# Kernel optimization log

Measured on AMD Instinct MI355X. Metric: run time of the kernel, lower is better.

The kernel has to match this reference:

```python
import jax, jax.numpy as jnp
import numpy as np

B = 256
LSTM = 512
FEAT = 3 * 3 * 512 + 16 + 8  # 4632
N_ACT = 4
ACT_SHAPE = 64
NUM_STEPS = 20
CANVAS_IN = 6 * 32 * 32  # 6144
H1 = int(FEAT / (FEAT / LSTM) ** (1.0 / 3.0))  # 2223
H2 = int(FEAT / (FEAT / LSTM) ** (2.0 / 3.0))  # 1067


def setup_inputs() -> dict:
    key = jax.random.key(0)
    ks = jax.random.split(key, 32)

    def g(k, shape, scale=0.02):
        return jax.random.normal(k, shape, dtype=jnp.float32) * scale

    inp = {
        "actualCanvas": jax.random.normal(ks[0], (B, 3, 32, 32), dtype=jnp.float32),
        "objectiveCanvas": jax.random.normal(ks[1], (B, 3, 32, 32), dtype=jnp.float32),
        "last_action_end_position": jax.random.randint(ks[2], (B,), 0, ACT_SHAPE),
        "episode_percentage": jax.random.randint(ks[3], (B,), 0, NUM_STEPS),
        # feature extractor stub (flatten -> linear -> relu), output 4608
        "Wfe": g(ks[4], (4608, CANVAS_IN)), "bfe": jnp.zeros((4608,), jnp.float32),
        "emb_end": g(ks[5], (ACT_SHAPE, 16), 1.0),
        "emb_ep": g(ks[6], (NUM_STEPS, 8), 1.0),
        "W1": g(ks[7], (H1, FEAT)), "b1": jnp.zeros((H1,), jnp.float32),
        "W2": g(ks[8], (H2, H1)), "b2": jnp.zeros((H2,), jnp.float32),
        "W3": g(ks[9], (LSTM, H2)), "b3": jnp.zeros((LSTM,), jnp.float32),
        "W_ih": g(ks[10], (4 * LSTM, LSTM)), "W_hh": g(ks[11], (4 * LSTM, LSTM)),
        "b_ih": jnp.zeros((4 * LSTM,), jnp.float32), "b_hh": jnp.zeros((4 * LSTM,), jnp.float32),
        "Wd1": g(ks[12], (N_ACT, LSTM // 2, LSTM)), "bd1": jnp.zeros((N_ACT, LSTM // 2), jnp.float32),
        "Wd2": g(ks[13], (N_ACT, ACT_SHAPE, LSTM // 2)), "bd2": jnp.zeros((N_ACT, ACT_SHAPE), jnp.float32),
        "emb_dec": g(ks[14], (N_ACT, ACT_SHAPE, 16), 1.0),
        "Wout": g(ks[15], (LSTM, LSTM + 16)), "bout": jnp.zeros((LSTM,), jnp.float32),
    }
    return inp


def reference(actualCanvas, objectiveCanvas, last_action_end_position, episode_percentage,
              Wfe, bfe, emb_end, emb_ep, W1, b1, W2, b2, W3, b3,
              W_ih, W_hh, b_ih, b_hh, Wd1, bd1, Wd2, bd2, emb_dec, Wout, bout):
    # feature extractor on channel-concatenated canvases -> [B, 4608]
    x = jnp.concatenate([actualCanvas, objectiveCanvas], axis=1).reshape(B, -1)
    fv = jax.nn.relu(x @ Wfe.T + bfe)
    feats = jnp.concatenate([fv, emb_end[last_action_end_position], emb_ep[episode_percentage]], axis=1)
    # fc1->fc2->fc3 (dropout = eval mode / identity)
    h = jax.nn.relu(feats @ W1.T + b1)
    h = jax.nn.relu(h @ W2.T + b2)
    h = jax.nn.relu(h @ W3.T + b3)  # [B, LSTM]
    # single-step LSTM with zero initial state (first execution)
    gates = h @ W_ih.T + b_ih + b_hh  # h0 = 0 so recurrent matmul vanishes
    i, f, g_, o = jnp.split(gates, 4, axis=1)
    c = jax.nn.sigmoid(i) * jnp.tanh(g_)
    seed = jax.nn.sigmoid(o) * jnp.tanh(c)  # [B, LSTM]
    z = seed
    log_probabilities = jnp.zeros((B,), jnp.float32)
    entropy = jnp.float32(0.0)
    actions = []
    base_key = jax.random.key(42)
    for k in range(N_ACT):
        hm = jax.nn.relu(z @ Wd1[k].T + bd1[k])
        logits = hm @ Wd2[k].T + bd2[k]  # [B, ACT_SHAPE]
        logp = jax.nn.log_softmax(logits, axis=1)
        probs = jnp.exp(logp)
        entropy = entropy + jnp.sum(-probs * logp)
        act = jax.random.categorical(jax.random.fold_in(base_key, k), logits, axis=1)  # [B]
        actions.append(act)
        log_probabilities = log_probabilities + jnp.take_along_axis(logp, act[:, None], axis=1)[:, 0]
        emb_a = emb_dec[k][act]  # [B,16]
        z = jax.nn.relu(jnp.concatenate([z, emb_a], axis=1) @ Wout.T + bout)
    action = jnp.stack(actions, axis=1)  # [B, N_ACT]
    return action, entropy, log_probabilities
```

## Files before the change

### kernel.cpp

```cpp
#include <hip/hip_runtime.h>
#include <hip/hip_bf16.h>
#include <stdint.h>

#define B_SZ   256
#define LSTM_N 512
#define FEAT_N 4632
#define FV_N   4608
#define CIN_N  6144
#define HALF_CIN 3072
#define ACT_N  64
#define LDSW   72
#define LD_FEAT 4672
#define LD_ZEXT 576

typedef __attribute__((ext_vector_type(8))) short bf16x8;
typedef __attribute__((ext_vector_type(4))) float f32x4;

#define BARRIER() asm volatile("s_waitcnt lgkmcnt(0)\ns_barrier" ::: "memory")

__device__ __forceinline__ short f2bf(float f) {
  uint32_t u = __float_as_uint(f);
  u += 0x7FFFu + ((u >> 16) & 1u);
  return (short)(u >> 16);
}
__device__ __forceinline__ float bf2f(short s) {
  return __uint_as_float(((uint32_t)(uint16_t)s) << 16);
}

__device__ __forceinline__ uint32_t rotl32(uint32_t x, int r) {
  return (x << r) | (x >> (32 - r));
}
__device__ __forceinline__ void threefry2x32(uint32_t k0, uint32_t k1,
                                             uint32_t x0, uint32_t x1,
                                             uint32_t& o0, uint32_t& o1) {
  uint32_t k2 = k0 ^ k1 ^ 0x1BD11BDAu;
  x0 += k0; x1 += k1;
  x0 += x1; x1 = rotl32(x1, 13); x1 ^= x0;
  x0 += x1; x1 = rotl32(x1, 15); x1 ^= x0;
  x0 += x1; x1 = rotl32(x1, 26); x1 ^= x0;
  x0 += x1; x1 = rotl32(x1,  6); x1 ^= x0;
  x0 += k1; x1 += k2 + 1u;
  x0 += x1; x1 = rotl32(x1, 17); x1 ^= x0;
  x0 += x1; x1 = rotl32(x1, 29); x1 ^= x0;
  x0 += x1; x1 = rotl32(x1, 16); x1 ^= x0;
  x0 += x1; x1 = rotl32(x1, 24); x1 ^= x0;
  x0 += k2; x1 += k0 + 2u;
  x0 += x1; x1 = rotl32(x1, 13); x1 ^= x0;
  x0 += x1; x1 = rotl32(x1, 15); x1 ^= x0;
  x0 += x1; x1 = rotl32(x1, 26); x1 ^= x0;
  x0 += x1; x1 = rotl32(x1,  6); x1 ^= x0;
  x0 += k0; x1 += k1 + 3u;
  x0 += x1; x1 = rotl32(x1, 17); x1 ^= x0;
  x0 += x1; x1 = rotl32(x1, 29); x1 ^= x0;
  x0 += x1; x1 = rotl32(x1, 16); x1 ^= x0;
  x0 += x1; x1 = rotl32(x1, 24); x1 ^= x0;
  x0 += k1; x1 += k2 + 4u;
  x0 += x1; x1 = rotl32(x1, 13); x1 ^= x0;
  x0 += x1; x1 = rotl32(x1, 15); x1 ^= x0;
  x0 += x1; x1 = rotl32(x1, 26); x1 ^= x0;
  x0 += x1; x1 = rotl32(x1,  6); x1 ^= x0;
  x0 += k2; x1 += k0 + 5u;
  o0 = x0; o1 = x1;
}

__global__ void concat_cvt_kernel(const float* __restrict__ act,
                                  const float* __restrict__ obj,
                                  short* __restrict__ xb) {
  int idx = blockIdx.x * 256 + threadIdx.x;
  if (idx >= B_SZ * 768) return;
  int row = idx / 768;
  int c8 = (idx - row * 768) * 8;
  const float* src = (c8 < HALF_CIN) ? (act + (size_t)row * HALF_CIN + c8)
                                     : (obj + (size_t)row * HALF_CIN + (c8 - HALF_CIN));
  float4 u = ((const float4*)src)[0];
  float4 v = ((const float4*)src)[1];
  bf16x8 r;
  r[0]=f2bf(u.x); r[1]=f2bf(u.y); r[2]=f2bf(u.z); r[3]=f2bf(u.w);
  r[4]=f2bf(v.x); r[5]=f2bf(v.y); r[6]=f2bf(v.z); r[7]=f2bf(v.w);
  *(bf16x8*)&xb[(size_t)row * CIN_N + c8] = r;
}

__global__ void gumbel_kernel(float* __restrict__ gum) {
  int idx = blockIdx.x * 256 + threadIdx.x;
  if (idx >= 4 * 16384) return;
  int k = idx >> 14;
  uint32_t j = (uint32_t)(idx & 16383);
  uint32_t f0, f1, o0, o1, bits;
  threefry2x32(0u, 42u, 0u, (uint32_t)k, f0, f1);
  if (j < 8192u) { threefry2x32(f0, f1, j, j + 8192u, o0, o1); bits = o0; }
  else           { threefry2x32(f0, f1, j - 8192u, j, o0, o1); bits = o1; }
  const float tiny = 1.17549435e-38f;
  float fu = __uint_as_float((bits >> 9) | 0x3f800000u) - 1.0f;
  float u = fmaxf(tiny, fu * (1.0f - tiny) + tiny);
  gum[idx] = -logf(-logf(u));
}

__global__ void fill_embs_kernel(const int* __restrict__ lastpos,
                                 const int* __restrict__ ep,
                                 const float* __restrict__ emb_end,
                                 const float* __restrict__ emb_ep,
                                 short* __restrict__ feats) {
  int b = blockIdx.x;
  int t = threadIdx.x;
  short* row = feats + (size_t)b * LD_FEAT;
  if (t < 16)      row[FV_N + t] = f2bf(emb_end[lastpos[b] * 16 + t]);
  else if (t < 24) row[FV_N + 16 + (t - 16)] = f2bf(emb_ep[ep[b] * 8 + (t - 16)]);
  else             row[FV_N + t] = 0;
}

__global__ __launch_bounds__(512) void gemm3_kernel(
    const short* __restrict__ A, int ldab,
    const float* __restrict__ W, int ldw,
    const float* __restrict__ bias1, const float* __restrict__ bias2,
    void* __restrict__ Cout, int ldc,
    short* __restrict__ P,
    int N, int K, int do_relu, int mode_f32, int kc, int nchunks) {
  __shared__ short Wlds[2][64 * LDSW];

  const int tid = threadIdx.x;
  const int w = tid >> 6, l = tid & 63, l15 = l & 15, lg = l >> 4;
  const int n0 = blockIdx.x * 64;
  const int Np = gridDim.x * 64;
  const int ks = blockIdx.y;
  const int kbeg = ks * kc;
  const int kend = (kbeg + kc < K) ? (kbeg + kc) : K;
  const int nk = (kend - kbeg + 63) >> 6;
  const bool wfast = ((ldw & 3) == 0);

  f32x4 acc[2][4];
#pragma unroll
  for (int i = 0; i < 2; ++i)
#pragma unroll
    for (int j = 0; j < 4; ++j) acc[i][j] = (f32x4){0.f, 0.f, 0.f, 0.f};

  const int wrow = tid >> 3, wq = tid & 7;
  float4 wrA[2], wrB[2], wrC[2], wrD[2];
  bf16x8 a0[4], a1[4];

  auto loadW = [&](float4* dst, int k0) {
    int gn = n0 + wrow; if (gn >= N) gn = N - 1;
    int gk = k0 + (wq << 3);
    const float* p = W + (size_t)gn * ldw + gk;
    if (wfast && (k0 + 64 <= K)) {
      dst[0] = ((const float4*)p)[0];
      dst[1] = ((const float4*)p)[1];
    } else {
      float t[8];
#pragma unroll
      for (int j = 0; j < 8; ++j) t[j] = (gk + j < K) ? p[j] : 0.f;
      dst[0] = (float4){t[0], t[1], t[2], t[3]};
      dst[1] = (float4){t[4], t[5], t[6], t[7]};
    }
  };
  auto storeW = [&](const float4* src, int buf) {
    short4 s0, s1;
    s0.x = f2bf(src[0].x); s0.y = f2bf(src[0].y);
    s0.z = f2bf(src[0].z); s0.w = f2bf(src[0].w);
    s1.x = f2bf(src[1].x); s1.y = f2bf(src[1].y);
    s1.z = f2bf(src[1].z); s1.w = f2bf(src[1].w);
    short* q = &Wlds[buf][wrow * LDSW + (wq << 3)];
    *(short4*)q = s0;
    *(short4*)(q + 4) = s1;
  };
  auto loadA = [&](bf16x8* dst, int k0) {
#pragma unroll
    for (int mi = 0; mi < 2; ++mi)
#pragma unroll
      for (int kh = 0; kh < 2; ++kh) {
        int m = (w << 5) + (mi << 4) + l15;
        int kk = k0 + (kh << 5) + (lg << 3);
        dst[(mi << 1) + kh] = *(const bf16x8*)&A[(size_t)m * ldab + kk];
      }
  };

#define MFMA_STEP(ACUR, BUF)                                                        \
  {                                                                                 \
    _Pragma("unroll")                                                               \
    for (int nj = 0; nj < 4; ++nj) {                                                \
      const short* bp = &Wlds[BUF][((nj << 4) + l15) * LDSW + (lg << 3)];           \
      bf16x8 b0 = *(const bf16x8*)bp;                                               \
      bf16x8 b1 = *(const bf16x8*)(bp + 32);                                        \
      acc[0][nj] = __builtin_amdgcn_mfma_f32_16x16x32_bf16(ACUR[0], b0, acc[0][nj], 0, 0, 0); \
      acc[1][nj] = __builtin_amdgcn_mfma_f32_16x16x32_bf16(ACUR[2], b0, acc[1][nj], 0, 0, 0); \
      acc[0][nj] = __builtin_amdgcn_mfma_f32_16x16x32_bf16(ACUR[1], b1, acc[0][nj], 0, 0, 0); \
      acc[1][nj] = __builtin_amdgcn_mfma_f32_16x16x32_bf16(ACUR[3], b1, acc[1][nj], 0, 0, 0); \
    }                                                                               \
  }

#define KSTEP(KT, WISS, WST, AC, AN, BUFC, BUFN)                      \
  {                                                                   \
    if ((KT) + 4 < nk) loadW(WISS, kbeg + (((KT) + 4) << 6));         \
    if ((KT) + 1 < nk) loadA(AN, kbeg + (((KT) + 1) << 6));           \
    MFMA_STEP(AC, BUFC);                                              \
    if ((KT) + 1 < nk) { storeW(WST, BUFN); BARRIER(); }              \
  }

  loadW(wrA, kbeg);
  if (nk > 1) loadW(wrB, kbeg + 64);
  if (nk > 2) loadW(wrC, kbeg + 128);
  if (nk > 3) loadW(wrD, kbeg + 192);
  loadA(a0, kbeg);
  storeW(wrA, 0);
  BARRIER();

  for (int kt = 0; kt < nk; kt += 4) {
    KSTEP(kt, wrA, wrB, a0, a1, 0, 1);
    if (kt + 1 < nk) KSTEP(kt + 1, wrB, wrC, a1, a0, 1, 0);
    if (kt + 2 < nk) KSTEP(kt + 2, wrC, wrD, a0, a1, 0, 1);
    if (kt + 3 < nk) KSTEP(kt + 3, wrD, wrA, a1, a0, 1, 0);
  }
#undef KSTEP
#undef MFMA_STEP

  if (nchunks == 1 && Cout) {
#pragma unroll
    for (int nj = 0; nj < 4; ++nj) {
      int gn = n0 + (nj << 4) + l15;
      float bsum = 0.f;
      if (gn < N) {
        if (bias1) bsum += bias1[gn];
        if (bias2) bsum += bias2[gn];
      }
#pragma unroll
      for (int mi = 0; mi < 2; ++mi)
#pragma unroll
        for (int r = 0; r < 4; ++r) {
          int gm = (w << 5) + (mi << 4) + (lg << 2) + r;
          float v = (gn < N) ? (acc[mi][nj][r] + bsum) : 0.f;
          if (do_relu) v = fmaxf(v, 0.f);
          if (mode_f32) ((float*)Cout)[(size_t)gm * ldc + gn] = v;
          else          ((short*)Cout)[(size_t)gm * ldc + gn] = f2bf(v);
        }
    }
  } else {
    short* Pb = P + (size_t)ks * 256 * Np;
#pragma unroll
    for (int nj = 0; nj < 4; ++nj) {
      int gn = n0 + (nj << 4) + l15;
#pragma unroll
      for (int mi = 0; mi < 2; ++mi)
#pragma unroll
        for (int r = 0; r < 4; ++r) {
          int gm = (w << 5) + (mi << 4) + (lg << 2) + r;
          Pb[(size_t)gm * Np + gn] = f2bf(acc[mi][nj][r]);
        }
    }
  }
}

__global__ void reduce_kernel(const short* __restrict__ P, int Np, int nchunks,
                              const float* __restrict__ bias1,
                              const float* __restrict__ bias2,
                              void* __restrict__ out, int ldc, int N,
                              int relu, int mode_f32) {
  int npack = Np >> 3;
  int idx = blockIdx.x * 256 + threadIdx.x;
  if (idx >= 256 * npack) return;
  int m = idx / npack;
  int n8 = (idx - m * npack) << 3;
  float s[8] = {0.f, 0.f, 0.f, 0.f, 0.f, 0.f, 0.f, 0.f};
  for (int ks = 0; ks < nchunks; ++ks) {
    bf16x8 v = *(const bf16x8*)&P[(size_t)ks * 256 * Np + (size_t)m * Np + n8];
#pragma unroll
    for (int j = 0; j < 8; ++j) s[j] += bf2f(v[j]);
  }
#pragma unroll
  for (int j = 0; j < 8; ++j) {
    int n = n8 + j;
    float r = 0.f;
    if (n < N) {
      r = s[j];
      if (bias1) r += bias1[n];
      if (bias2) r += bias2[n];
      if (relu) r = fmaxf(r, 0.f);
    }
    s[j] = r;
  }
  if (mode_f32) {
    float* o = (float*)out + (size_t)m * ldc + n8;
#pragma unroll
    for (int j = 0; j < 8; ++j) o[j] = s[j];
  } else {
    bf16x8 r;
#pragma unroll
    for (int j = 0; j < 8; ++j) r[j] = f2bf(s[j]);
    *(bf16x8*)((short*)out + (size_t)m * ldc + n8) = r;
  }
}

__global__ void reduce_lstm_kernel(const short* __restrict__ P, int nchunks,
                                   const float* __restrict__ b_ih,
                                   const float* __restrict__ b_hh,
                                   short* __restrict__ zext) {
  int idx = blockIdx.x * 256 + threadIdx.x;
  if (idx >= 256 * 64) return;
  int m = idx >> 6;
  int n8 = (idx & 63) << 3;
  float gi[8] = {}, gg[8] = {}, go[8] = {};
  for (int ks = 0; ks < nchunks; ++ks) {
    const short* base = P + ((size_t)ks * 256 + m) * 2048;
    bf16x8 vi = *(const bf16x8*)(base + n8);
    bf16x8 vg = *(const bf16x8*)(base + 1024 + n8);
    bf16x8 vo = *(const bf16x8*)(base + 1536 + n8);
#pragma unroll
    for (int j = 0; j < 8; ++j) {
      gi[j] += bf2f(vi[j]); gg[j] += bf2f(vg[j]); go[j] += bf2f(vo[j]);
    }
  }
  bf16x8 hv;
#pragma unroll
  for (int j = 0; j < 8; ++j) {
    int n = n8 + j;
    float i_ = gi[j] + b_ih[n] + b_hh[n];
    float g_ = gg[j] + b_ih[1024 + n] + b_hh[1024 + n];
    float o_ = go[j] + b_ih[1536 + n] + b_hh[1536 + n];
    float si = 1.f / (1.f + expf(-i_));
    float so = 1.f / (1.f + expf(-o_));
    float c = si * tanhf(g_);
    hv[j] = f2bf(so * tanhf(c));
  }
  *(bf16x8*)&zext[(size_t)m * LD_ZEXT + n8] = hv;
}

__global__ __launch_bounds__(256) void logits_sample_kernel(
    const short* __restrict__ hm,
    const float* __restrict__ Wd2k,
    const float* __restrict__ bd2k,
    const float* __restrict__ gumk,
    const float* __restrict__ embk,
    short* __restrict__ zext,
    int* __restrict__ act_out, float* __restrict__ logp_out,
    float* __restrict__ ent_out, int write_emb) {
  __shared__ short Wl[64 * 264];
  const int tid = threadIdx.x;
  const int w = tid >> 6, l = tid & 63, l15 = l & 15, lg = l >> 4;
  const int mbase = blockIdx.x * 64 + w * 16;

  {
    int r = tid >> 2;
    int c0 = (tid & 3) << 6;
    const float* src = Wd2k + r * 256 + c0;
    short* dst = &Wl[r * 264 + c0];
#pragma unroll
    for (int i = 0; i < 8; ++i) {
      float4 u = ((const float4*)src)[2 * i];
      float4 v = ((const float4*)src)[2 * i + 1];
      bf16x8 t;
      t[0]=f2bf(u.x); t[1]=f2bf(u.y); t[2]=f2bf(u.z); t[3]=f2bf(u.w);
      t[4]=f2bf(v.x); t[5]=f2bf(v.y); t[6]=f2bf(v.z); t[7]=f2bf(v.w);
      *(bf16x8*)(dst + 8 * i) = t;
    }
  }
  __syncthreads();

  f32x4 acc[4];
#pragma unroll
  for (int j = 0; j < 4; ++j) acc[j] = (f32x4){0.f, 0.f, 0.f, 0.f};

#pragma unroll
  for (int kt = 0; kt < 4; ++kt) {
    int k0 = kt << 6;
    const short* arow = &hm[(size_t)(mbase + l15) * 256 + k0 + (lg << 3)];
    bf16x8 af0 = *(const bf16x8*)arow;
    bf16x8 af1 = *(const bf16x8*)(arow + 32);
#pragma unroll
    for (int nj = 0; nj < 4; ++nj) {
      const short* bp = &Wl[((nj << 4) + l15) * 264 + k0 + (lg << 3)];
      bf16x8 b0 = *(const bf16x8*)bp;
      bf16x8 b1 = *(const bf16x8*)(bp + 32);
      acc[nj] = __builtin_amdgcn_mfma_f32_16x16x32_bf16(af0, b0, acc[nj], 0, 0, 0);
      acc[nj] = __builtin_amdgcn_mfma_f32_16x16x32_bf16(af1, b1, acc[nj], 0, 0, 0);
    }
  }

  float bcol[4];
#pragma unroll
  for (int nj = 0; nj < 4; ++nj) bcol[nj] = bd2k[(nj << 4) + l15];

#pragma unroll
  for (int r = 0; r < 4; ++r) {
    int row = mbase + (lg << 2) + r;
    float lv[4];
#pragma unroll
    for (int nj = 0; nj < 4; ++nj) lv[nj] = acc[nj][r] + bcol[nj];
    float mx = fmaxf(fmaxf(lv[0], lv[1]), fmaxf(lv[2], lv[3]));
#pragma unroll
    for (int off = 8; off; off >>= 1) mx = fmaxf(mx, __shfl_xor(mx, off));
    float es = expf(lv[0]-mx) + expf(lv[1]-mx) + expf(lv[2]-mx) + expf(lv[3]-mx);
#pragma unroll
    for (int off = 8; off; off >>= 1) es += __shfl_xor(es, off);
    float lse = logf(es);
    float lp[4], ent = 0.f;
#pragma unroll
    for (int nj = 0; nj < 4; ++nj) {
      lp[nj] = lv[nj] - mx - lse;
      ent += -expf(lp[nj]) * lp[nj];
    }
#pragma unroll
    for (int off = 8; off; off >>= 1) ent += __shfl_xor(ent, off);
    float bv = -3.4e38f; int bc = 64; float blp = 0.f;
#pragma unroll
    for (int nj = 0; nj < 4; ++nj) {
      int col = (nj << 4) + l15;
      float pert = lv[nj] + gumk[row * 64 + col];
      if (pert > bv || (pert == bv && col < bc)) { bv = pert; bc = col; blp = lp[nj]; }
    }
#pragma unroll
    for (int off = 8; off; off >>= 1) {
      float ov = __shfl_xor(bv, off);
      int oc = __shfl_xor(bc, off);
      float olp = __shfl_xor(blp, off);
      if (ov > bv || (ov == bv && oc < bc)) { bv = ov; bc = oc; blp = olp; }
    }
    if (l15 == 0) {
      act_out[row] = bc;
      logp_out[row] = blp;
      ent_out[row] = ent;
    }
    if (write_emb) {
      short* zr = zext + (size_t)row * LD_ZEXT;
      zr[512 + l15] = f2bf(embk[bc * 16 + l15]);
      zr[528 + l15] = 0;
      zr[544 + l15] = 0;
      zr[560 + l15] = 0;
    }
  }
}

__global__ void finalize_kernel(const int* __restrict__ act,
                                const float* __restrict__ logp_k,
                                const float* __restrict__ ent,
                                float* __restrict__ out) {
  __shared__ float sred[4];
  int t = threadIdx.x;
#pragma unroll
  for (int k = 0; k < 4; ++k)
    out[t * 4 + k] = (float)act[k * 256 + t];
  float lp = 0.f;
#pragma unroll
  for (int k = 0; k < 4; ++k) lp += logp_k[k * 256 + t];
  out[1025 + t] = lp;

  float v = 0.f;
#pragma unroll
  for (int k = 0; k < 4; ++k) v += ent[k * 256 + t];
#pragma unroll
  for (int off = 32; off; off >>= 1) v += __shfl_xor(v, off);
  if ((t & 63) == 0) sred[t >> 6] = v;
  __syncthreads();
  if (t == 0) out[1024] = sred[0] + sred[1] + sred[2] + sred[3];
}

extern "C" void kernel_launch(void* const* d_in, const int* in_sizes, int n_in,
                              void* d_out, int out_size, void* d_ws, size_t ws_size,
                              hipStream_t stream) {
  float* out = (float*)d_out;
  char* out_bytes = (char*)d_out;
  auto sentinel = [&](int code) { hipMemsetAsync(out_bytes + 4096, code, 4, stream); };

  if (n_in < 25 || in_sizes[0] != B_SZ * 3 * 32 * 32 ||
      in_sizes[4] != FV_N * CIN_N || in_sizes[23] != LSTM_N * 528 ||
      in_sizes[9] <= 0 || in_sizes[9] > 8192 ||
      in_sizes[11] <= 0 || in_sizes[11] > 8192) {
    sentinel(0x42);
    return;
  }

  const float* actual = (const float*)d_in[0];
  const float* object = (const float*)d_in[1];
  const int* lastpos  = (const int*)d_in[2];
  const int* ep       = (const int*)d_in[3];
  const float* Wfe    = (const float*)d_in[4];
  const float* bfe    = (const float*)d_in[5];
  const float* emb_end= (const float*)d_in[6];
  const float* emb_ep = (const float*)d_in[7];
  const float* W1     = (const float*)d_in[8];
  const float* b1     = (const float*)d_in[9];
  const float* W2     = (const float*)d_in[10];
  const float* b2     = (const float*)d_in[11];
  const float* W3     = (const float*)d_in[12];
  const float* b3     = (const float*)d_in[13];
  const float* W_ih   = (const float*)d_in[14];
  const float* b_ih   = (const float*)d_in[16];
  const float* b_hh   = (const float*)d_in[17];
  const float* Wd1    = (const float*)d_in[18];
  const float* bd1    = (const float*)d_in[19];
  const float* Wd2    = (const float*)d_in[20];
  const float* bd2    = (const float*)d_in[21];
  const float* embdec = (const float*)d_in[22];
  const float* Wout   = (const float*)d_in[23];
  const float* bout   = (const float*)d_in[24];

  const int H1 = in_sizes[9];
  const int H2 = in_sizes[11];
  const int ldh1 = 64 * ((H1 + 63) / 64);
  const int ldh2 = 64 * ((H2 + 63) / 64);

  char* wsb = (char*)d_ws;
  size_t off = 0;
  auto alloc = [&](size_t bytes) {
    char* p = wsb + off;
    off += (bytes + 255) & ~(size_t)255;
    return p;
  };
  float* logpk = (float*)alloc(1024 * 4);
  float* entk  = (float*)alloc(1024 * 4);
  int*   actk  = (int*)alloc(1024 * 4);
  float* gumb  = (float*)alloc(4 * 16384 * 4);
  short* xb    = (short*)alloc((size_t)B_SZ * CIN_N * 2);
  short* feats = (short*)alloc((size_t)B_SZ * LD_FEAT * 2);
  short* h1    = (short*)alloc((size_t)B_SZ * ldh1 * 2);
  short* h2    = (short*)alloc((size_t)B_SZ * ldh2 * 2);
  short* h3    = (short*)alloc((size_t)B_SZ * 512 * 2);
  short* zextA = (short*)alloc((size_t)B_SZ * LD_ZEXT * 2);
  short* zextB = (short*)alloc((size_t)B_SZ * LD_ZEXT * 2);
  short* hm    = (short*)alloc((size_t)B_SZ * 256 * 2);
  if (off + (4 << 20) > ws_size) {
    sentinel(0x43);
    return;
  }
  short* slab = (short*)(wsb + off);
  const size_t slab_bytes = ws_size - off;

  auto gemm = [&](const short* A, int ldab, const float* W, int ldw,
                  const float* bb1, const float* bb2,
                  void* C, int ldc, int N, int K, int relu, int mode_f32,
                  bool split, int fuse) {
    int nblk = (N + 63) / 64;
    int Np = nblk * 64;
    int chunks = 1;
    int kc = 64 * ((K + 63) / 64);
    if (split) {
      int c = (640 + nblk - 1) / nblk;
      int capk = K >> 7; if (capk < 1) capk = 1;
      if (c > capk) c = capk;
      size_t cap = slab_bytes / ((size_t)256 * Np * 2);
      if ((size_t)c > cap) c = (int)cap;
      if (c < 1) c = 1;
      kc = 64 * ((K + 64 * c - 1) / (64 * c));
      chunks = (K + kc - 1) / kc;
    }
    dim3 g(nblk, chunks);
    void* Ck = (fuse == 1) ? nullptr : C;
    gemm3_kernel<<<g, dim3(512), 0, stream>>>(
        A, ldab, W, ldw, bb1, bb2, Ck, ldc, slab, N, K, relu, mode_f32, kc, chunks);
    if (fuse == 1) {
      reduce_lstm_kernel<<<dim3(64), dim3(256), 0, stream>>>(
          slab, chunks, bb1, bb2, (short*)C);
    } else if (chunks > 1) {
      int npack = Np >> 3;
      reduce_kernel<<<dim3((256 * npack + 255) / 256), dim3(256), 0, stream>>>(
          slab, Np, chunks, bb1, bb2, C, ldc, N, relu, mode_f32);
    }
  };

  concat_cvt_kernel<<<dim3(768), dim3(256), 0, stream>>>(actual, object, xb);
  gumbel_kernel<<<dim3(256), dim3(256), 0, stream>>>(gumb);
  gemm(xb, CIN_N, Wfe, CIN_N, bfe, nullptr, feats, LD_FEAT, FV_N, CIN_N, 1, 0, true, 0);
  fill_embs_kernel<<<dim3(B_SZ), dim3(64), 0, stream>>>(lastpos, ep, emb_end, emb_ep, feats);
  gemm(feats, LD_FEAT, W1, FEAT_N, b1, nullptr, h1, ldh1, H1, FEAT_N, 1, 0, true, 0);
  gemm(h1, ldh1, W2, H1, b2, nullptr, h2, ldh2, H2, H1, 1, 0, true, 0);
  gemm(h2, ldh2, W3, H2, b3, nullptr, h3, 512, LSTM_N, H2, 1, 0, true, 0);
  gemm(h3, 512, W_ih, LSTM_N, b_ih, b_hh, zextA, LD_ZEXT, 4 * LSTM_N, LSTM_N, 0, 0, true, 1);

  short* zcur = zextA;
  short* znxt = zextB;
  for (int k = 0; k < 4; ++k) {
    const float* Wd1k = Wd1 + (size_t)k * 256 * LSTM_N;
    const float* bd1k = bd1 + (size_t)k * 256;
    const float* Wd2k = Wd2 + (size_t)k * ACT_N * 256;
    const float* bd2k = bd2 + (size_t)k * ACT_N;
    const float* embk = embdec + (size_t)k * ACT_N * 16;
    gemm(zcur, LD_ZEXT, Wd1k, LSTM_N, bd1k, nullptr, hm, 256, 256, LSTM_N, 1, 0, false, 0);
    logits_sample_kernel<<<dim3(4), dim3(256), 0, stream>>>(
        hm, Wd2k, bd2k, gumb + k * 16384, embk, zcur,
        actk + k * B_SZ, logpk + k * B_SZ, entk + k * B_SZ, (k < 3) ? 1 : 0);
    if (k < 3) {
      gemm(zcur, LD_ZEXT, Wout, 528, bout, nullptr, znxt, LD_ZEXT, LSTM_N, 528, 1, 0, false, 0);
      short* t = zcur; zcur = znxt; znxt = t;
    }
  }

  finalize_kernel<<<dim3(1), dim3(256), 0, stream>>>(actk, logpk, entk, out);
}
```

Measured before the change: 319.8 us.

## Restructure GEMM K-loop into four-buffer LDS batches and retune split-K

Replaces the double-buffered LDS weight pipeline, which stored one tile and hit a barrier after every 64-wide K step, with a four-buffer scheme. Four weight tiles are prefetched into registers, four MFMA steps run from LDS, and all four tiles are then stored between two barriers. This cuts barriers per K step. The cost is more LDS per block, which may lower occupancy, and a longer stall at each batch boundary. The split-K heuristic also changes to target more blocks with larger minimum chunks (K>>8 cap), so each chunk spans enough K tiles to fill the batches.

Result: faster. 310.1 us (-3.0%).

```diff
diff --git a/kernel.cpp b/kernel.cpp
--- a/kernel.cpp
+++ b/kernel.cpp
@@ -115,7 +115,7 @@
     void* __restrict__ Cout, int ldc,
     short* __restrict__ P,
     int N, int K, int do_relu, int mode_f32, int kc, int nchunks) {
-  __shared__ short Wlds[2][64 * LDSW];
+  __shared__ short Wlds[4][64 * LDSW];
 
   const int tid = threadIdx.x;
   const int w = tid >> 6, l = tid & 63, l15 = l & 15, lg = l >> 4;
@@ -134,7 +134,7 @@
     for (int j = 0; j < 4; ++j) acc[i][j] = (f32x4){0.f, 0.f, 0.f, 0.f};
 
   const int wrow = tid >> 3, wq = tid & 7;
-  float4 wrA[2], wrB[2], wrC[2], wrD[2];
+  float4 wr0[2], wr1[2], wr2[2], wr3[2];
   bf16x8 a0[4], a1[4];
 
   auto loadW = [&](float4* dst, int k0) {
@@ -187,29 +187,47 @@
     }                                                                               \
   }
 
-#define KSTEP(KT, WISS, WST, AC, AN, BUFC, BUFN)                      \
-  {                                                                   \
-    if ((KT) + 4 < nk) loadW(WISS, kbeg + (((KT) + 4) << 6));         \
-    if ((KT) + 1 < nk) loadA(AN, kbeg + (((KT) + 1) << 6));           \
-    MFMA_STEP(AC, BUFC);                                              \
-    if ((KT) + 1 < nk) { storeW(WST, BUFN); BARRIER(); }              \
-  }
-
-  loadW(wrA, kbeg);
-  if (nk > 1) loadW(wrB, kbeg + 64);
-  if (nk > 2) loadW(wrC, kbeg + 128);
-  if (nk > 3) loadW(wrD, kbeg + 192);
+  if (0 < nk) loadW(wr0, kbeg);
+  if (1 < nk) loadW(wr1, kbeg + 64);
+  if (2 < nk) loadW(wr2, kbeg + 128);
+  if (3 < nk) loadW(wr3, kbeg + 192);
   loadA(a0, kbeg);
-  storeW(wrA, 0);
+  if (0 < nk) storeW(wr0, 0);
+  if (1 < nk) storeW(wr1, 1);
+  if (2 < nk) storeW(wr2, 2);
+  if (3 < nk) storeW(wr3, 3);
   BARRIER();
 
-  for (int kt = 0; kt < nk; kt += 4) {
-    KSTEP(kt, wrA, wrB, a0, a1, 0, 1);
-    if (kt + 1 < nk) KSTEP(kt + 1, wrB, wrC, a1, a0, 1, 0);
-    if (kt + 2 < nk) KSTEP(kt + 2, wrC, wrD, a0, a1, 0, 1);
-    if (kt + 3 < nk) KSTEP(kt + 3, wrD, wrA, a1, a0, 1, 0);
-  }
-#undef KSTEP
+  for (int b = 0; b < nk; b += 4) {
+    if (b + 4 < nk) loadW(wr0, kbeg + ((b + 4) << 6));
+    if (b + 5 < nk) loadW(wr1, kbeg + ((b + 5) << 6));
+    if (b + 6 < nk) loadW(wr2, kbeg + ((b + 6) << 6));
+    if (b + 7 < nk) loadW(wr3, kbeg + ((b + 7) << 6));
+    {
+      if (b + 1 < nk) loadA(a1, kbeg + ((b + 1) << 6));
+      MFMA_STEP(a0, 0);
+    }
+    if (b + 1 < nk) {
+      if (b + 2 < nk) loadA(a0, kbeg + ((b + 2) << 6));
+      MFMA_STEP(a1, 1);
+    }
+    if (b + 2 < nk) {
+      if (b + 3 < nk) loadA(a1, kbeg + ((b + 3) << 6));
+      MFMA_STEP(a0, 2);
+    }
+    if (b + 3 < nk) {
+      if (b + 4 < nk) loadA(a0, kbeg + ((b + 4) << 6));
+      MFMA_STEP(a1, 3);
+    }
+    if (b + 4 < nk) {
+      BARRIER();
+      storeW(wr0, 0);
+      if (b + 5 < nk) storeW(wr1, 1);
+      if (b + 6 < nk) storeW(wr2, 2);
+      if (b + 7 < nk) storeW(wr3, 3);
+      BARRIER();
+    }
+  }
 #undef MFMA_STEP
 
   if (nchunks == 1 && Cout) {
@@ -531,8 +549,8 @@
     int chunks = 1;
     int kc = 64 * ((K + 63) / 64);
     if (split) {
-      int c = (640 + nblk - 1) / nblk;
-      int capk = K >> 7; if (capk < 1) capk = 1;
+      int c = (768 + nblk - 1) / nblk;
+      int capk = K >> 8; if (capk < 1) capk = 1;
       if (c > capk) c = capk;
       size_t cap = slab_bytes / ((size_t)256 * Np * 2);
       if ((size_t)c > cap) c = (int)cap;
```

## Replace LDS-staged GEMM with register-direct weight loads and wider split-K

Applied to the files above, without the earlier changes.

The GEMM kernel no longer stages fp32 weights through double-buffered LDS with barriers. Each wave now loads and converts its weight fragments straight from global memory into registers and computes a 64x64 tile with 4 waves of 256 threads. The split-K target rises from 640 to 1536 blocks and the chunk count is now capped by the number of K tiles. The small decoder GEMMs also switch to split-K with a separate reduce pass. This is meant to remove barrier and LDS overhead and raise parallelism for the bandwidth-bound weight streaming. The cost is that each wave rereads the weight rows with no prefetch pipelining, and extra reduce launches are added for the tiny decoder GEMMs.

Result: slower. 377.6 us (+18.1%).

```diff
diff --git a/kernel.cpp b/kernel.cpp
--- a/kernel.cpp
+++ b/kernel.cpp
@@ -9,14 +9,11 @@
 #define CIN_N  6144
 #define HALF_CIN 3072
 #define ACT_N  64
-#define LDSW   72
 #define LD_FEAT 4672
 #define LD_ZEXT 576
 
 typedef __attribute__((ext_vector_type(8))) short bf16x8;
 typedef __attribute__((ext_vector_type(4))) float f32x4;
-
-#define BARRIER() asm volatile("s_waitcnt lgkmcnt(0)\ns_barrier" ::: "memory")
 
 __device__ __forceinline__ short f2bf(float f) {
   uint32_t u = __float_as_uint(f);
@@ -108,109 +105,73 @@
   else             row[FV_N + t] = 0;
 }
 
-__global__ __launch_bounds__(512) void gemm3_kernel(
+__global__ __launch_bounds__(256, 3) void gemm4_kernel(
     const short* __restrict__ A, int ldab,
     const float* __restrict__ W, int ldw,
     const float* __restrict__ bias1, const float* __restrict__ bias2,
     void* __restrict__ Cout, int ldc,
     short* __restrict__ P,
     int N, int K, int do_relu, int mode_f32, int kc, int nchunks) {
-  __shared__ short Wlds[2][64 * LDSW];
-
   const int tid = threadIdx.x;
-  const int w = tid >> 6, l = tid & 63, l15 = l & 15, lg = l >> 4;
+  const int wv = tid >> 6, l = tid & 63, l15 = l & 15, lg = l >> 4;
   const int n0 = blockIdx.x * 64;
   const int Np = gridDim.x * 64;
   const int ks = blockIdx.y;
   const int kbeg = ks * kc;
   const int kend = (kbeg + kc < K) ? (kbeg + kc) : K;
-  const int nk = (kend - kbeg + 63) >> 6;
-  const bool wfast = ((ldw & 3) == 0);
-
-  f32x4 acc[2][4];
-#pragma unroll
-  for (int i = 0; i < 2; ++i)
+  const bool wal = ((ldw & 3) == 0);
+  const int mrow = wv << 6;
+
+  f32x4 acc[4][4];
+#pragma unroll
+  for (int i = 0; i < 4; ++i)
 #pragma unroll
     for (int j = 0; j < 4; ++j) acc[i][j] = (f32x4){0.f, 0.f, 0.f, 0.f};
 
-  const int wrow = tid >> 3, wq = tid & 7;
-  float4 wrA[2], wrB[2], wrC[2], wrD[2];
-  bf16x8 a0[4], a1[4];
-
-  auto loadW = [&](float4* dst, int k0) {
-    int gn = n0 + wrow; if (gn >= N) gn = N - 1;
-    int gk = k0 + (wq << 3);
-    const float* p = W + (size_t)gn * ldw + gk;
-    if (wfast && (k0 + 64 <= K)) {
-      dst[0] = ((const float4*)p)[0];
-      dst[1] = ((const float4*)p)[1];
-    } else {
-      float t[8];
-#pragma unroll
-      for (int j = 0; j < 8; ++j) t[j] = (gk + j < K) ? p[j] : 0.f;
-      dst[0] = (float4){t[0], t[1], t[2], t[3]};
-      dst[1] = (float4){t[4], t[5], t[6], t[7]};
-    }
-  };
-  auto storeW = [&](const float4* src, int buf) {
-    short4 s0, s1;
-    s0.x = f2bf(src[0].x); s0.y = f2bf(src[0].y);
-    s0.z = f2bf(src[0].z); s0.w = f2bf(src[0].w);
-    s1.x = f2bf(src[1].x); s1.y = f2bf(src[1].y);
-    s1.z = f2bf(src[1].z); s1.w = f2bf(src[1].w);
-    short* q = &Wlds[buf][wrow * LDSW + (wq << 3)];
-    *(short4*)q = s0;
-    *(short4*)(q + 4) = s1;
-  };
-  auto loadA = [&](bf16x8* dst, int k0) {
-#pragma unroll
-    for (int mi = 0; mi < 2; ++mi)
-#pragma unroll
-      for (int kh = 0; kh < 2; ++kh) {
-        int m = (w << 5) + (mi << 4) + l15;
-        int kk = k0 + (kh << 5) + (lg << 3);
-        dst[(mi << 1) + kh] = *(const bf16x8*)&A[(size_t)m * ldab + kk];
+  int gnc[4];
+#pragma unroll
+  for (int nj = 0; nj < 4; ++nj) {
+    int gn = n0 + (nj << 4) + l15;
+    gnc[nj] = (gn < N) ? gn : (N - 1);
+  }
+
+  for (int kt = kbeg; kt < kend; kt += 64) {
+    bf16x8 af[4][2];
+#pragma unroll
+    for (int mf = 0; mf < 4; ++mf)
+#pragma unroll
+      for (int kh = 0; kh < 2; ++kh)
+        af[mf][kh] = *(const bf16x8*)&A[(size_t)(mrow + (mf << 4) + l15) * ldab +
+                                        kt + (kh << 5) + (lg << 3)];
+    const bool fast = wal && (kt + 64 <= K);
+#pragma unroll
+    for (int nj = 0; nj < 4; ++nj) {
+      const float* wp = W + (size_t)gnc[nj] * ldw + kt + (lg << 3);
+      bf16x8 b0, b1;
+      if (fast) {
+        float4 u0 = ((const float4*)wp)[0];
+        float4 u1 = ((const float4*)wp)[1];
+        float4 v0 = ((const float4*)(wp + 32))[0];
+        float4 v1 = ((const float4*)(wp + 32))[1];
+        b0[0]=f2bf(u0.x); b0[1]=f2bf(u0.y); b0[2]=f2bf(u0.z); b0[3]=f2bf(u0.w);
+        b0[4]=f2bf(u1.x); b0[5]=f2bf(u1.y); b0[6]=f2bf(u1.z); b0[7]=f2bf(u1.w);
+        b1[0]=f2bf(v0.x); b1[1]=f2bf(v0.y); b1[2]=f2bf(v0.z); b1[3]=f2bf(v0.w);
+        b1[4]=f2bf(v1.x); b1[5]=f2bf(v1.y); b1[6]=f2bf(v1.z); b1[7]=f2bf(v1.w);
+      } else {
+        int kk = kt + (lg << 3);
+#pragma unroll
+        for (int j = 0; j < 8; ++j) {
+          b0[j] = (kk + j < K) ? f2bf(wp[j]) : (short)0;
+          b1[j] = (kk + 32 + j < K) ? f2bf(wp[32 + j]) : (short)0;
+        }
       }
-  };
-
-#define MFMA_STEP(ACUR, BUF)                                                        \
-  {                                                                                 \
-    _Pragma("unroll")                                                               \
-    for (int nj = 0; nj < 4; ++nj) {                                                \
-      const short* bp = &Wlds[BUF][((nj << 4) + l15) * LDSW + (lg << 3)];           \
-      bf16x8 b0 = *(const bf16x8*)bp;                                               \
-      bf16x8 b1 = *(const bf16x8*)(bp + 32);                                        \
-      acc[0][nj] = __builtin_amdgcn_mfma_f32_16x16x32_bf16(ACUR[0], b0, acc[0][nj], 0, 0, 0); \
-      acc[1][nj] = __builtin_amdgcn_mfma_f32_16x16x32_bf16(ACUR[2], b0, acc[1][nj], 0, 0, 0); \
-      acc[0][nj] = __builtin_amdgcn_mfma_f32_16x16x32_bf16(ACUR[1], b1, acc[0][nj], 0, 0, 0); \
-      acc[1][nj] = __builtin_amdgcn_mfma_f32_16x16x32_bf16(ACUR[3], b1, acc[1][nj], 0, 0, 0); \
-    }                                                                               \
-  }
-
-#define KSTEP(KT, WISS, WST, AC, AN, BUFC, BUFN)                      \
-  {                                                                   \
-    if ((KT) + 4 < nk) loadW(WISS, kbeg + (((KT) + 4) << 6));         \
-    if ((KT) + 1 < nk) loadA(AN, kbeg + (((KT) + 1) << 6));           \
-    MFMA_STEP(AC, BUFC);                                              \
-    if ((KT) + 1 < nk) { storeW(WST, BUFN); BARRIER(); }              \
-  }
-
-  loadW(wrA, kbeg);
-  if (nk > 1) loadW(wrB, kbeg + 64);
-  if (nk > 2) loadW(wrC, kbeg + 128);
-  if (nk > 3) loadW(wrD, kbeg + 192);
-  loadA(a0, kbeg);
-  storeW(wrA, 0);
-  BARRIER();
-
-  for (int kt = 0; kt < nk; kt += 4) {
-    KSTEP(kt, wrA, wrB, a0, a1, 0, 1);
-    if (kt + 1 < nk) KSTEP(kt + 1, wrB, wrC, a1, a0, 1, 0);
-    if (kt + 2 < nk) KSTEP(kt + 2, wrC, wrD, a0, a1, 0, 1);
-    if (kt + 3 < nk) KSTEP(kt + 3, wrD, wrA, a1, a0, 1, 0);
-  }
-#undef KSTEP
-#undef MFMA_STEP
+#pragma unroll
+      for (int mf = 0; mf < 4; ++mf) {
+        acc[mf][nj] = __builtin_amdgcn_mfma_f32_16x16x32_bf16(af[mf][0], b0, acc[mf][nj], 0, 0, 0);
+        acc[mf][nj] = __builtin_amdgcn_mfma_f32_16x16x32_bf16(af[mf][1], b1, acc[mf][nj], 0, 0, 0);
+      }
+    }
+  }
 
   if (nchunks == 1 && Cout) {
 #pragma unroll
@@ -222,11 +183,11 @@
         if (bias2) bsum += bias2[gn];
       }
 #pragma unroll
-      for (int mi = 0; mi < 2; ++mi)
+      for (int mf = 0; mf < 4; ++mf)
 #pragma unroll
         for (int r = 0; r < 4; ++r) {
-          int gm = (w << 5) + (mi << 4) + (lg << 2) + r;
-          float v = (gn < N) ? (acc[mi][nj][r] + bsum) : 0.f;
+          int gm = mrow + (mf << 4) + (lg << 2) + r;
+          float v = (gn < N) ? (acc[mf][nj][r] + bsum) : 0.f;
           if (do_relu) v = fmaxf(v, 0.f);
           if (mode_f32) ((float*)Cout)[(size_t)gm * ldc + gn] = v;
           else          ((short*)Cout)[(size_t)gm * ldc + gn] = f2bf(v);
@@ -238,11 +199,11 @@
     for (int nj = 0; nj < 4; ++nj) {
       int gn = n0 + (nj << 4) + l15;
 #pragma unroll
-      for (int mi = 0; mi < 2; ++mi)
+      for (int mf = 0; mf < 4; ++mf)
 #pragma unroll
         for (int r = 0; r < 4; ++r) {
-          int gm = (w << 5) + (mi << 4) + (lg << 2) + r;
-          Pb[(size_t)gm * Np + gn] = f2bf(acc[mi][nj][r]);
+          int gm = mrow + (mf << 4) + (lg << 2) + r;
+          Pb[(size_t)gm * Np + gn] = f2bf(acc[mf][nj][r]);
         }
     }
   }
@@ -529,20 +490,21 @@
     int nblk = (N + 63) / 64;
     int Np = nblk * 64;
     int chunks = 1;
-    int kc = 64 * ((K + 63) / 64);
+    int tiles = (K + 63) / 64;
+    int kc = 64 * tiles;
     if (split) {
-      int c = (640 + nblk - 1) / nblk;
-      int capk = K >> 7; if (capk < 1) capk = 1;
-      if (c > capk) c = capk;
+      int c = (1536 + nblk - 1) / nblk;
+      if (c > tiles) c = tiles;
       size_t cap = slab_bytes / ((size_t)256 * Np * 2);
       if ((size_t)c > cap) c = (int)cap;
       if (c < 1) c = 1;
-      kc = 64 * ((K + 64 * c - 1) / (64 * c));
-      chunks = (K + kc - 1) / kc;
+      int ct = (tiles + c - 1) / c;
+      kc = 64 * ct;
+      chunks = (tiles + ct - 1) / ct;
     }
     dim3 g(nblk, chunks);
     void* Ck = (fuse == 1) ? nullptr : C;
-    gemm3_kernel<<<g, dim3(512), 0, stream>>>(
+    gemm4_kernel<<<g, dim3(256), 0, stream>>>(
         A, ldab, W, ldw, bb1, bb2, Ck, ldc, slab, N, K, relu, mode_f32, kc, chunks);
     if (fuse == 1) {
       reduce_lstm_kernel<<<dim3(64), dim3(256), 0, stream>>>(
@@ -571,12 +533,12 @@
     const float* Wd2k = Wd2 + (size_t)k * ACT_N * 256;
     const float* bd2k = bd2 + (size_t)k * ACT_N;
     const float* embk = embdec + (size_t)k * ACT_N * 16;
-    gemm(zcur, LD_ZEXT, Wd1k, LSTM_N, bd1k, nullptr, hm, 256, 256, LSTM_N, 1, 0, false, 0);
+    gemm(zcur, LD_ZEXT, Wd1k, LSTM_N, bd1k, nullptr, hm, 256, 256, LSTM_N, 1, 0, true, 0);
     logits_sample_kernel<<<dim3(4), dim3(256), 0, stream>>>(
         hm, Wd2k, bd2k, gumb + k * 16384, embk, zcur,
         actk + k * B_SZ, logpk + k * B_SZ, entk + k * B_SZ, (k < 3) ? 1 : 0);
     if (k < 3) {
-      gemm(zcur, LD_ZEXT, Wout, 528, bout, nullptr, znxt, LD_ZEXT, LSTM_N, 528, 1, 0, false, 0);
+      gemm(zcur, LD_ZEXT, Wout, 528, bout, nullptr, znxt, LD_ZEXT, LSTM_N, 528, 1, 0, true, 0);
       short* t = zcur; zcur = znxt; znxt = t;
     }
   }
```
